# Kernel optimization log

Hardware: AMD Instinct MI355X
Metric: run time of the kernel (lower is better)

Reference implementation:

```python
import jax, jax.numpy as jnp
import numpy as np

B, D1, T = 256, 512, 256   # batch, input features, time steps
O1, O2 = 256, 128          # output features, output time/classes


def setup_inputs() -> dict:
    key = jax.random.key(0)
    ks = jax.random.split(key, 5)
    x = jax.random.normal(ks[0], (B, D1, T), dtype=jnp.float32)
    W1 = jax.random.normal(ks[1], (O1, D1), dtype=jnp.float32) / np.sqrt(D1).astype(np.float32)
    W = jax.random.normal(ks[2], (T, T), dtype=jnp.float32) / np.sqrt(T).astype(np.float32)
    W2 = jax.random.normal(ks[3], (T, O2), dtype=jnp.float32) / np.sqrt(T).astype(np.float32)
    alpha = jnp.array([0.5], dtype=jnp.float32)
    bias = jax.random.normal(ks[4], (O1, O2), dtype=jnp.float32) * 0.01
    return {"x": x, "W1": W1, "W": W, "W2": W2, "alpha": alpha, "bias": bias}


def reference(x, W1, W, W2, alpha, bias):
    # mode-1 product: project features. E: [B, O1, T]
    E = jnp.einsum('od,bdt->bot', W1, x)
    # temporal attention: softmax over time of E @ W. A: [B, O1, T]
    A = jax.nn.softmax(jnp.einsum('bot,ts->bos', E, W), axis=-1)
    a = alpha[0]
    blended = a * E + (1.0 - a) * E * A
    # mode-2 product: project time axis, add bias. Y: [B, O1, O2]
    Y = jnp.einsum('bot,ts->bos', blended, W2) + bias
    # per-sample softmax over the output-feature axis (torch.softmax(item4[i], 0))
    return jax.nn.softmax(Y, axis=1)
```

## Files before the change

kernel.cpp:

```cpp
#include <hip/hip_runtime.h>
#include <hip/hip_bf16.h>
#include <math.h>

#define B_   256
#define D1_  512
#define T_   256
#define O1_  256
#define O2_  128
#define OT   128

typedef __attribute__((ext_vector_type(8))) _Float16 f16x8;
typedef __attribute__((ext_vector_type(2))) _Float16 f16x2;
typedef __attribute__((ext_vector_type(4))) float f32x4;

__device__ inline unsigned pkh2(float a, float b) {
    union { f16x2 h; unsigned u; } c;
    c.h.x = (_Float16)a; c.h.y = (_Float16)b;
    return c.u;
}

__device__ inline void splith4(float v0, float v1, float v2, float v3,
                               uint2& hp, uint2& lp) {
    _Float16 h0 = (_Float16)v0, h1 = (_Float16)v1;
    _Float16 h2 = (_Float16)v2, h3 = (_Float16)v3;
    float r0 = v0 - (float)h0, r1 = v1 - (float)h1;
    float r2 = v2 - (float)h2, r3 = v3 - (float)h3;
    union { f16x2 h; unsigned u; } c;
    c.h.x = h0; c.h.y = h1; hp.x = c.u;
    c.h.x = h2; c.h.y = h3; hp.y = c.u;
    lp.x = pkh2(r0, r1); lp.y = pkh2(r2, r3);
}

__device__ inline uint2 cvth4(float v0, float v1, float v2, float v3) {
    uint2 r; r.x = pkh2(v0, v1); r.y = pkh2(v2, v3); return r;
}

__device__ inline f16x8 cvt8h(float4 a, float4 b) {
    f16x8 r;
    r[0] = (_Float16)a.x; r[1] = (_Float16)a.y;
    r[2] = (_Float16)a.z; r[3] = (_Float16)a.w;
    r[4] = (_Float16)b.x; r[5] = (_Float16)b.y;
    r[6] = (_Float16)b.z; r[7] = (_Float16)b.w;
    return r;
}

__device__ inline f16x8 ld16(const char* p) {
    union { uint2 a[2]; f16x8 v; } f;
    f.a[0] = *(const uint2*)p;
    f.a[1] = *(const uint2*)(p + 8);
    return f.v;
}
__device__ inline f16x8 ldb128(const char* p) { return *(const f16x8*)p; }

#define MFMAH __builtin_amdgcn_mfma_f32_16x16x32_f16

__global__ __launch_bounds__(1024, 4) void tabl_mfma(
    const float* __restrict__ x, const float* __restrict__ W1,
    const float* __restrict__ W, const float* __restrict__ W2,
    const float* __restrict__ alpha, const float* __restrict__ bias,
    float* __restrict__ out)
{
    __shared__ __align__(16) char Eh[OT * 512];
    __shared__ __align__(16) char Bst[2][2][256 * 72];
    __shared__ float redm[4][OT];
    __shared__ float reds[4][OT];

    const int tid    = threadIdx.x;
    const int lane16 = tid & 15;
    const int lg     = (tid >> 4) & 3;
    const int wid    = tid >> 6;
    const int wm     = wid >> 2;
    const int wn     = wid & 3;

    const int bi  = blockIdx.x;
    const int xcd = bi & 7, q = bi >> 3;
    const int b     = xcd + (q >> 1) * 8;
    const int obase = (q & 1) * OT;

    const int xs_t = tid & 255;
    const int koct = tid >> 8;
    const int stO  = xs_t * 72 + koct * 16;
    const int zs = tid & 127, zoct = (tid >> 7) & 7;
    const int stZ  = zs * 72 + zoct * 8;

    const int rArow[2] = { obase + wm * 32 + lane16, obase + wm * 32 + 16 + lane16 };
    const int eR[2]    = { wm * 32 + lane16, wm * 32 + 16 + lane16 };
    const int eBase[2] = { eR[0] * 512, eR[1] * 512 };
    const int eSw[2]   = { (eR[0] & 7) << 4, (eR[1] & 7) << 4 };
    int bOff[4], b3Off[2];
    #pragma unroll
    for (int nt = 0; nt < 4; ++nt) bOff[nt] = (wn * 64 + nt * 16 + lane16) * 72 + lg * 16;
    #pragma unroll
    for (int nt = 0; nt < 2; ++nt) b3Off[nt] = (wn * 32 + nt * 16 + lane16) * 72 + lg * 16;

    f32x4 Eacc[2][4];
    #pragma unroll
    for (int mt = 0; mt < 2; ++mt)
        #pragma unroll
        for (int nt = 0; nt < 4; ++nt) Eacc[mt][nt] = (f32x4){0.f,0.f,0.f,0.f};

    const float* xcol = x + (size_t)b * (D1_ * T_) + xs_t;
    float xr[8]; float4 apf[2][2];

    {
        #pragma unroll
        for (int j = 0; j < 8; ++j) xr[j] = xcol[(size_t)(koct * 8 + j) * T_];
        #pragma unroll
        for (int mt = 0; mt < 2; ++mt) {
            const float4* ap = (const float4*)(W1 + (size_t)rArow[mt] * D1_ + lg * 8);
            apf[mt][0] = ap[0]; apf[mt][1] = ap[1];
        }
        uint2 hp, lp;
        splith4(xr[0],xr[1],xr[2],xr[3],hp,lp);
        *(uint2*)(Bst[0][0] + stO) = hp; *(uint2*)(Bst[0][1] + stO) = lp;
        splith4(xr[4],xr[5],xr[6],xr[7],hp,lp);
        *(uint2*)(Bst[0][0] + stO + 8) = hp; *(uint2*)(Bst[0][1] + stO + 8) = lp;
    }
    __syncthreads();

    #pragma unroll 2
    for (int c = 0; c < 16; ++c) {
        const int cur = c & 1;
        if (c < 15) {
            #pragma unroll
            for (int j = 0; j < 8; ++j)
                xr[j] = xcol[(size_t)((c + 1) * 32 + koct * 8 + j) * T_];
        }
        f16x8 Ah[2];
        #pragma unroll
        for (int mt = 0; mt < 2; ++mt) Ah[mt] = cvt8h(apf[mt][0], apf[mt][1]);
        if (c < 15) {
            #pragma unroll
            for (int mt = 0; mt < 2; ++mt) {
                const float4* ap = (const float4*)(W1 + (size_t)rArow[mt] * D1_ + (c + 1) * 32 + lg * 8);
                apf[mt][0] = ap[0]; apf[mt][1] = ap[1];
            }
        }
        __builtin_amdgcn_s_setprio(1);
        #pragma unroll
        for (int np = 0; np < 2; ++np) {
            f16x8 Bh[2], Bl[2];
            #pragma unroll
            for (int h = 0; h < 2; ++h) {
                Bh[h] = ld16(Bst[cur][0] + bOff[np * 2 + h]);
                Bl[h] = ld16(Bst[cur][1] + bOff[np * 2 + h]);
            }
            #pragma unroll
            for (int mt = 0; mt < 2; ++mt)
                #pragma unroll
                for (int h = 0; h < 2; ++h) {
                    Eacc[mt][np*2+h] = MFMAH(Ah[mt], Bh[h], Eacc[mt][np*2+h], 0,0,0);
                    Eacc[mt][np*2+h] = MFMAH(Ah[mt], Bl[h], Eacc[mt][np*2+h], 0,0,0);
                }
        }
        __builtin_amdgcn_s_setprio(0);
        if (c < 15) {
            uint2 hp, lp;
            splith4(xr[0],xr[1],xr[2],xr[3],hp,lp);
            *(uint2*)(Bst[cur^1][0] + stO) = hp; *(uint2*)(Bst[cur^1][1] + stO) = lp;
            splith4(xr[4],xr[5],xr[6],xr[7],hp,lp);
            *(uint2*)(Bst[cur^1][0] + stO + 8) = hp; *(uint2*)(Bst[cur^1][1] + stO + 8) = lp;
        }
        __syncthreads();
    }

    #pragma unroll
    for (int mt = 0; mt < 2; ++mt)
        #pragma unroll
        for (int nt = 0; nt < 4; ++nt)
            #pragma unroll
            for (int i = 0; i < 4; ++i) {
                int r = wm * 32 + mt * 16 + lg * 4 + i;
                int t = wn * 64 + nt * 16 + lane16;
                union { _Float16 h; unsigned short u; } cc;
                cc.h = (_Float16)Eacc[mt][nt][i];
                *(unsigned short*)(Eh + r * 512 + ((2 * t) ^ ((r & 7) << 4))) = cc.u;
            }

    f32x4 Sacc[2][4];
    #pragma unroll
    for (int mt = 0; mt < 2; ++mt)
        #pragma unroll
        for (int nt = 0; nt < 4; ++nt) Sacc[mt][nt] = (f32x4){0.f,0.f,0.f,0.f};

    const float* wcol = W + xs_t;
    float wr[8];
    {
        #pragma unroll
        for (int j = 0; j < 8; ++j) wr[j] = wcol[(size_t)(koct * 8 + j) * T_];
        *(uint2*)(Bst[0][0] + stO)     = cvth4(wr[0],wr[1],wr[2],wr[3]);
        *(uint2*)(Bst[0][0] + stO + 8) = cvth4(wr[4],wr[5],wr[6],wr[7]);
    }
    __syncthreads();

    #pragma unroll 2
    for (int c = 0; c < 8; ++c) {
        const int cur = c & 1;
        if (c < 7) {
            #pragma unroll
            for (int j = 0; j < 8; ++j)
                wr[j] = wcol[(size_t)((c + 1) * 32 + koct * 8 + j) * T_];
        }
        f16x8 Af[2];
        #pragma unroll
        for (int mt = 0; mt < 2; ++mt)
            Af[mt] = ldb128(Eh + eBase[mt] + ((c * 64 + lg * 16) ^ eSw[mt]));
        __builtin_amdgcn_s_setprio(1);
        #pragma unroll
        for (int np = 0; np < 2; ++np) {
            f16x8 Bf[2];
            #pragma unroll
            for (int h = 0; h < 2; ++h) Bf[h] = ld16(Bst[cur][0] + bOff[np * 2 + h]);
            #pragma unroll
            for (int mt = 0; mt < 2; ++mt)
                #pragma unroll
                for (int h = 0; h < 2; ++h)
                    Sacc[mt][np*2+h] = MFMAH(Af[mt], Bf[h], Sacc[mt][np*2+h], 0,0,0);
        }
        __builtin_amdgcn_s_setprio(0);
        if (c < 7) {
            *(uint2*)(Bst[cur^1][0] + stO)     = cvth4(wr[0],wr[1],wr[2],wr[3]);
            *(uint2*)(Bst[cur^1][0] + stO + 8) = cvth4(wr[4],wr[5],wr[6],wr[7]);
        }
        __syncthreads();
    }

    const float a_ = alpha[0];
    float pm[2][4];
    #pragma unroll
    for (int mt = 0; mt < 2; ++mt)
        #pragma unroll
        for (int i = 0; i < 4; ++i) {
            float m = fmaxf(fmaxf(Sacc[mt][0][i], Sacc[mt][1][i]),
                            fmaxf(Sacc[mt][2][i], Sacc[mt][3][i]));
            m = fmaxf(m, __shfl_xor(m, 1));
            m = fmaxf(m, __shfl_xor(m, 2));
            m = fmaxf(m, __shfl_xor(m, 4));
            m = fmaxf(m, __shfl_xor(m, 8));
            float s = 0.f;
            #pragma unroll
            for (int nt = 0; nt < 4; ++nt) {
                float p = __expf(Sacc[mt][nt][i] - m);
                Sacc[mt][nt][i] = p; s += p;
            }
            s += __shfl_xor(s, 1);
            s += __shfl_xor(s, 2);
            s += __shfl_xor(s, 4);
            s += __shfl_xor(s, 8);
            pm[mt][i] = m;
            if (lane16 == 0) {
                int r = wm * 32 + mt * 16 + lg * 4 + i;
                redm[wn][r] = m; reds[wn][r] = s;
            }
        }
    float zr[4];
    #pragma unroll
    for (int j = 0; j < 4; ++j) zr[j] = W2[(size_t)(zoct * 4 + j) * O2_ + zs];
    __syncthreads();

    #pragma unroll
    for (int mt = 0; mt < 2; ++mt)
        #pragma unroll
        for (int i = 0; i < 4; ++i) {
            int r = wm * 32 + mt * 16 + lg * 4 + i;
            float M = fmaxf(fmaxf(redm[0][r], redm[1][r]),
                            fmaxf(redm[2][r], redm[3][r]));
            float den = reds[0][r] * __expf(redm[0][r] - M)
                      + reds[1][r] * __expf(redm[1][r] - M)
                      + reds[2][r] * __expf(redm[2][r] - M)
                      + reds[3][r] * __expf(redm[3][r] - M);
            float sc = __expf(pm[mt][i] - M) / den;
            #pragma unroll
            for (int nt = 0; nt < 4; ++nt) {
                float f = a_ + (1.f - a_) * Sacc[mt][nt][i] * sc;
                float v = Eacc[mt][nt][i] * f;
                int t = wn * 64 + nt * 16 + lane16;
                union { _Float16 h; unsigned short u; } cc;
                cc.h = (_Float16)v;
                *(unsigned short*)(Eh + r * 512 + ((2 * t) ^ ((r & 7) << 4))) = cc.u;
            }
        }
    {
        *(uint2*)(Bst[0][0] + stZ) = cvth4(zr[0], zr[1], zr[2], zr[3]);
    }
    __syncthreads();

    f32x4 Yacc[2][2];
    #pragma unroll
    for (int mt = 0; mt < 2; ++mt)
        #pragma unroll
        for (int nt = 0; nt < 2; ++nt) Yacc[mt][nt] = (f32x4){0.f,0.f,0.f,0.f};

    #pragma unroll 2
    for (int c = 0; c < 8; ++c) {
        const int cur = c & 1;
        if (c < 7) {
            #pragma unroll
            for (int j = 0; j < 4; ++j)
                zr[j] = W2[(size_t)((c + 1) * 32 + zoct * 4 + j) * O2_ + zs];
        }
        f16x8 Ahf[2];
        #pragma unroll
        for (int mt = 0; mt < 2; ++mt)
            Ahf[mt] = ldb128(Eh + eBase[mt] + ((c * 64 + lg * 16) ^ eSw[mt]));
        __builtin_amdgcn_s_setprio(1);
        {
            f16x8 Bh[2];
            #pragma unroll
            for (int nt = 0; nt < 2; ++nt) Bh[nt] = ld16(Bst[cur][0] + b3Off[nt]);
            #pragma unroll
            for (int mt = 0; mt < 2; ++mt)
                #pragma unroll
                for (int nt = 0; nt < 2; ++nt)
                    Yacc[mt][nt] = MFMAH(Ahf[mt], Bh[nt], Yacc[mt][nt], 0,0,0);
        }
        __builtin_amdgcn_s_setprio(0);
        if (c < 7) {
            *(uint2*)(Bst[cur^1][0] + stZ) = cvth4(zr[0], zr[1], zr[2], zr[3]);
        }
        __syncthreads();
    }

    #pragma unroll
    for (int mt = 0; mt < 2; ++mt)
        #pragma unroll
        for (int nt = 0; nt < 2; ++nt)
            #pragma unroll
            for (int i = 0; i < 4; ++i) {
                int o  = obase + wm * 32 + mt * 16 + lg * 4 + i;
                int s2 = wn * 32 + nt * 16 + lane16;
                out[((size_t)b * O1_ + o) * O2_ + s2] =
                    Yacc[mt][nt][i] + bias[(size_t)o * O2_ + s2];
            }
}

__global__ __launch_bounds__(256) void softmax_o1(float* __restrict__ out)
{
    __shared__ float sm[2][128], ss[2][128];
    const int b  = blockIdx.x;
    const int s2 = threadIdx.x & 127;
    const int oh = threadIdx.x >> 7;
    float* p = out + (size_t)b * (O1_ * O2_) + s2;
    float m = -INFINITY, s = 0.f;
    #pragma unroll 4
    for (int o = oh * 128; o < oh * 128 + 128; ++o) {
        float v = p[(size_t)o * O2_];
        float mn = fmaxf(m, v);
        s = s * __expf(m - mn) + __expf(v - mn);
        m = mn;
    }
    sm[oh][s2] = m; ss[oh][s2] = s;
    __syncthreads();
    float M = fmaxf(sm[0][s2], sm[1][s2]);
    float S = ss[0][s2] * __expf(sm[0][s2] - M) + ss[1][s2] * __expf(sm[1][s2] - M);
    float inv = 1.f / S;
    #pragma unroll 4
    for (int o = oh * 128; o < oh * 128 + 128; ++o) {
        float v = p[(size_t)o * O2_];
        p[(size_t)o * O2_] = __expf(v - M) * inv;
    }
}

extern "C" void kernel_launch(void* const* d_in, const int* in_sizes, int n_in,
                              void* d_out, int out_size, void* d_ws, size_t ws_size,
                              hipStream_t stream)
{
    const float* x     = (const float*)d_in[0];
    const float* W1    = (const float*)d_in[1];
    const float* W     = (const float*)d_in[2];
    const float* W2    = (const float*)d_in[3];
    const float* alpha = (const float*)d_in[4];
    const float* bias  = (const float*)d_in[5];
    float* out = (float*)d_out;

    tabl_mfma<<<dim3(512), 1024, 0, stream>>>(x, W1, W, W2, alpha, bias, out);
    softmax_o1<<<B_, 256, 0, stream>>>(out);
}
```

Before: 139.8 us.

## Prefetch global operands two chunks ahead across all three GEMM stages

Deepens the software pipeline in the three GEMM loops (x/W1 projection, E@W scores, blended@W2). Global loads for chunk c+2 are now issued while chunk c is computed, and the LDS store of the already-loaded chunk c+1 happens at the top of the iteration instead of after the MFMAs. This is meant to hide more global memory latency behind MFMA work. The cost is more live registers for the extra prefetch buffers, which could lower occupancy.

```diff
diff --git a/kernel.cpp b/kernel.cpp
--- a/kernel.cpp
+++ b/kernel.cpp
@@ -100,20 +100,23 @@
         for (int nt = 0; nt < 4; ++nt) Eacc[mt][nt] = (f32x4){0.f,0.f,0.f,0.f};
 
     const float* xcol = x + (size_t)b * (D1_ * T_) + xs_t;
-    float xr[8]; float4 apf[2][2];
+    float xrN[8]; float4 apfC[2][2], apfN[2][2];
 
     {
-        #pragma unroll
-        for (int j = 0; j < 8; ++j) xr[j] = xcol[(size_t)(koct * 8 + j) * T_];
+        float x0[8];
+        #pragma unroll
+        for (int j = 0; j < 8; ++j) x0[j] = xcol[(size_t)(koct * 8 + j) * T_];
         #pragma unroll
         for (int mt = 0; mt < 2; ++mt) {
             const float4* ap = (const float4*)(W1 + (size_t)rArow[mt] * D1_ + lg * 8);
-            apf[mt][0] = ap[0]; apf[mt][1] = ap[1];
-        }
+            apfC[mt][0] = ap[0]; apfC[mt][1] = ap[1];
+        }
+        #pragma unroll
+        for (int j = 0; j < 8; ++j) xrN[j] = xcol[(size_t)(32 + koct * 8 + j) * T_];
         uint2 hp, lp;
-        splith4(xr[0],xr[1],xr[2],xr[3],hp,lp);
+        splith4(x0[0],x0[1],x0[2],x0[3],hp,lp);
         *(uint2*)(Bst[0][0] + stO) = hp; *(uint2*)(Bst[0][1] + stO) = lp;
-        splith4(xr[4],xr[5],xr[6],xr[7],hp,lp);
+        splith4(x0[4],x0[5],x0[6],x0[7],hp,lp);
         *(uint2*)(Bst[0][0] + stO + 8) = hp; *(uint2*)(Bst[0][1] + stO + 8) = lp;
     }
     __syncthreads();
@@ -122,18 +125,25 @@
     for (int c = 0; c < 16; ++c) {
         const int cur = c & 1;
         if (c < 15) {
+            uint2 hp, lp;
+            splith4(xrN[0],xrN[1],xrN[2],xrN[3],hp,lp);
+            *(uint2*)(Bst[cur^1][0] + stO) = hp; *(uint2*)(Bst[cur^1][1] + stO) = lp;
+            splith4(xrN[4],xrN[5],xrN[6],xrN[7],hp,lp);
+            *(uint2*)(Bst[cur^1][0] + stO + 8) = hp; *(uint2*)(Bst[cur^1][1] + stO + 8) = lp;
+        }
+        if (c < 14) {
             #pragma unroll
             for (int j = 0; j < 8; ++j)
-                xr[j] = xcol[(size_t)((c + 1) * 32 + koct * 8 + j) * T_];
+                xrN[j] = xcol[(size_t)((c + 2) * 32 + koct * 8 + j) * T_];
         }
         f16x8 Ah[2];
         #pragma unroll
-        for (int mt = 0; mt < 2; ++mt) Ah[mt] = cvt8h(apf[mt][0], apf[mt][1]);
+        for (int mt = 0; mt < 2; ++mt) Ah[mt] = cvt8h(apfC[mt][0], apfC[mt][1]);
         if (c < 15) {
             #pragma unroll
             for (int mt = 0; mt < 2; ++mt) {
                 const float4* ap = (const float4*)(W1 + (size_t)rArow[mt] * D1_ + (c + 1) * 32 + lg * 8);
-                apf[mt][0] = ap[0]; apf[mt][1] = ap[1];
+                apfN[mt][0] = ap[0]; apfN[mt][1] = ap[1];
             }
         }
         __builtin_amdgcn_s_setprio(1);
@@ -154,12 +164,9 @@
                 }
         }
         __builtin_amdgcn_s_setprio(0);
-        if (c < 15) {
-            uint2 hp, lp;
-            splith4(xr[0],xr[1],xr[2],xr[3],hp,lp);
-            *(uint2*)(Bst[cur^1][0] + stO) = hp; *(uint2*)(Bst[cur^1][1] + stO) = lp;
-            splith4(xr[4],xr[5],xr[6],xr[7],hp,lp);
-            *(uint2*)(Bst[cur^1][0] + stO + 8) = hp; *(uint2*)(Bst[cur^1][1] + stO + 8) = lp;
+        #pragma unroll
+        for (int mt = 0; mt < 2; ++mt) {
+            apfC[mt][0] = apfN[mt][0]; apfC[mt][1] = apfN[mt][1];
         }
         __syncthreads();
     }
@@ -184,12 +191,15 @@
         for (int nt = 0; nt < 4; ++nt) Sacc[mt][nt] = (f32x4){0.f,0.f,0.f,0.f};
 
     const float* wcol = W + xs_t;
-    float wr[8];
+    float wrN[8];
     {
-        #pragma unroll
-        for (int j = 0; j < 8; ++j) wr[j] = wcol[(size_t)(koct * 8 + j) * T_];
-        *(uint2*)(Bst[0][0] + stO)     = cvth4(wr[0],wr[1],wr[2],wr[3]);
-        *(uint2*)(Bst[0][0] + stO + 8) = cvth4(wr[4],wr[5],wr[6],wr[7]);
+        float w0[8];
+        #pragma unroll
+        for (int j = 0; j < 8; ++j) w0[j] = wcol[(size_t)(koct * 8 + j) * T_];
+        #pragma unroll
+        for (int j = 0; j < 8; ++j) wrN[j] = wcol[(size_t)(32 + koct * 8 + j) * T_];
+        *(uint2*)(Bst[0][0] + stO)     = cvth4(w0[0],w0[1],w0[2],w0[3]);
+        *(uint2*)(Bst[0][0] + stO + 8) = cvth4(w0[4],w0[5],w0[6],w0[7]);
     }
     __syncthreads();
 
@@ -197,9 +207,13 @@
     for (int c = 0; c < 8; ++c) {
         const int cur = c & 1;
         if (c < 7) {
+            *(uint2*)(Bst[cur^1][0] + stO)     = cvth4(wrN[0],wrN[1],wrN[2],wrN[3]);
+            *(uint2*)(Bst[cur^1][0] + stO + 8) = cvth4(wrN[4],wrN[5],wrN[6],wrN[7]);
+        }
+        if (c < 6) {
             #pragma unroll
             for (int j = 0; j < 8; ++j)
-                wr[j] = wcol[(size_t)((c + 1) * 32 + koct * 8 + j) * T_];
+                wrN[j] = wcol[(size_t)((c + 2) * 32 + koct * 8 + j) * T_];
         }
         f16x8 Af[2];
         #pragma unroll
@@ -218,10 +232,6 @@
                     Sacc[mt][np*2+h] = MFMAH(Af[mt], Bf[h], Sacc[mt][np*2+h], 0,0,0);
         }
         __builtin_amdgcn_s_setprio(0);
-        if (c < 7) {
-            *(uint2*)(Bst[cur^1][0] + stO)     = cvth4(wr[0],wr[1],wr[2],wr[3]);
-            *(uint2*)(Bst[cur^1][0] + stO + 8) = cvth4(wr[4],wr[5],wr[6],wr[7]);
-        }
         __syncthreads();
     }
 
@@ -253,9 +263,11 @@
                 redm[wn][r] = m; reds[wn][r] = s;
             }
         }
-    float zr[4];
-    #pragma unroll
-    for (int j = 0; j < 4; ++j) zr[j] = W2[(size_t)(zoct * 4 + j) * O2_ + zs];
+    float zr0[4], zrN[4];
+    #pragma unroll
+    for (int j = 0; j < 4; ++j) zr0[j] = W2[(size_t)(zoct * 4 + j) * O2_ + zs];
+    #pragma unroll
+    for (int j = 0; j < 4; ++j) zrN[j] = W2[(size_t)(32 + zoct * 4 + j) * O2_ + zs];
     __syncthreads();
 
     #pragma unroll
@@ -281,7 +293,7 @@
             }
         }
     {
-        *(uint2*)(Bst[0][0] + stZ) = cvth4(zr[0], zr[1], zr[2], zr[3]);
+        *(uint2*)(Bst[0][0] + stZ) = cvth4(zr0[0], zr0[1], zr0[2], zr0[3]);
     }
     __syncthreads();
 
@@ -295,9 +307,12 @@
     for (int c = 0; c < 8; ++c) {
         const int cur = c & 1;
         if (c < 7) {
+            *(uint2*)(Bst[cur^1][0] + stZ) = cvth4(zrN[0], zrN[1], zrN[2], zrN[3]);
+        }
+        if (c < 6) {
             #pragma unroll
             for (int j = 0; j < 4; ++j)
-                zr[j] = W2[(size_t)((c + 1) * 32 + zoct * 4 + j) * O2_ + zs];
+                zrN[j] = W2[(size_t)((c + 2) * 32 + zoct * 4 + j) * O2_ + zs];
         }
         f16x8 Ahf[2];
         #pragma unroll
@@ -315,9 +330,6 @@
                     Yacc[mt][nt] = MFMAH(Ahf[mt], Bh[nt], Yacc[mt][nt], 0,0,0);
         }
         __builtin_amdgcn_s_setprio(0);
-        if (c < 7) {
-            *(uint2*)(Bst[cur^1][0] + stZ) = cvth4(zr[0], zr[1], zr[2], zr[3]);
-        }
         __syncthreads();
     }
 
```

New measurement: 147.4 us. 1.05x slower.

## Drop split-fp16 x compensation and halve per-block output rows

Applied to the files above, without the earlier changes.

The first GEMM no longer splits x into high and low fp16 halves, so the second compensating MFMA and its staging buffer are removed. Each block now covers 64 output rows with 512 threads over 1024 blocks, which halves shared memory per block and changes the occupancy and work split. The blend step reads E back from shared memory instead of from the accumulator registers. This cuts MFMA work and register pressure, but with 1024 blocks each batch's x slice is reloaded by four blocks instead of two, and dropping the compensation lowers the precision of E.

```diff
diff --git a/kernel.cpp b/kernel.cpp
--- a/kernel.cpp
+++ b/kernel.cpp
@@ -7,43 +7,24 @@
 #define T_   256
 #define O1_  256
 #define O2_  128
-#define OT   128
+#define OT   64
 
 typedef __attribute__((ext_vector_type(8))) _Float16 f16x8;
-typedef __attribute__((ext_vector_type(2))) _Float16 f16x2;
 typedef __attribute__((ext_vector_type(4))) float f32x4;
 
 __device__ inline unsigned pkh2(float a, float b) {
-    union { f16x2 h; unsigned u; } c;
-    c.h.x = (_Float16)a; c.h.y = (_Float16)b;
-    return c.u;
-}
-
-__device__ inline void splith4(float v0, float v1, float v2, float v3,
-                               uint2& hp, uint2& lp) {
-    _Float16 h0 = (_Float16)v0, h1 = (_Float16)v1;
-    _Float16 h2 = (_Float16)v2, h3 = (_Float16)v3;
-    float r0 = v0 - (float)h0, r1 = v1 - (float)h1;
-    float r2 = v2 - (float)h2, r3 = v3 - (float)h3;
-    union { f16x2 h; unsigned u; } c;
-    c.h.x = h0; c.h.y = h1; hp.x = c.u;
-    c.h.x = h2; c.h.y = h3; hp.y = c.u;
-    lp.x = pkh2(r0, r1); lp.y = pkh2(r2, r3);
-}
-
+    union { _Float16 h[2]; unsigned u; } c;
+    c.h[0] = (_Float16)a; c.h[1] = (_Float16)b; return c.u;
+}
 __device__ inline uint2 cvth4(float v0, float v1, float v2, float v3) {
     uint2 r; r.x = pkh2(v0, v1); r.y = pkh2(v2, v3); return r;
 }
-
-__device__ inline f16x8 cvt8h(float4 a, float4 b) {
+__device__ inline f16x8 cvt8h(const float* v) {
     f16x8 r;
-    r[0] = (_Float16)a.x; r[1] = (_Float16)a.y;
-    r[2] = (_Float16)a.z; r[3] = (_Float16)a.w;
-    r[4] = (_Float16)b.x; r[5] = (_Float16)b.y;
-    r[6] = (_Float16)b.z; r[7] = (_Float16)b.w;
+    #pragma unroll
+    for (int j = 0; j < 8; ++j) r[j] = (_Float16)v[j];
     return r;
 }
-
 __device__ inline f16x8 ld16(const char* p) {
     union { uint2 a[2]; f16x8 v; } f;
     f.a[0] = *(const uint2*)p;
@@ -54,14 +35,14 @@
 
 #define MFMAH __builtin_amdgcn_mfma_f32_16x16x32_f16
 
-__global__ __launch_bounds__(1024, 4) void tabl_mfma(
+__global__ __launch_bounds__(512, 4) void tabl_mfma(
     const float* __restrict__ x, const float* __restrict__ W1,
     const float* __restrict__ W, const float* __restrict__ W2,
     const float* __restrict__ alpha, const float* __restrict__ bias,
     float* __restrict__ out)
 {
     __shared__ __align__(16) char Eh[OT * 512];
-    __shared__ __align__(16) char Bst[2][2][256 * 72];
+    __shared__ __align__(16) char Bst[2][256 * 72];
     __shared__ float redm[4][OT];
     __shared__ float reds[4][OT];
 
@@ -72,16 +53,16 @@
     const int wm     = wid >> 2;
     const int wn     = wid & 3;
 
-    const int bi  = blockIdx.x;
-    const int xcd = bi & 7, q = bi >> 3;
-    const int b     = xcd + (q >> 1) * 8;
-    const int obase = (q & 1) * OT;
-
-    const int xs_t = tid & 255;
-    const int koct = tid >> 8;
-    const int stO  = xs_t * 72 + koct * 16;
-    const int zs = tid & 127, zoct = (tid >> 7) & 7;
-    const int stZ  = zs * 72 + zoct * 8;
+    const int bid = blockIdx.x;
+    const int idx = bid >> 3;
+    const int b     = (bid & 7) + 8 * (idx >> 2);
+    const int obase = (idx & 3) * OT;
+
+    const int xs_t  = tid & 255;
+    const int xs_kh = tid >> 8;
+    const int stO   = xs_t * 72 + xs_kh * 32;
+    const int zs = tid & 127, zq = (tid >> 7) & 3;
+    const int stZ   = zs * 72 + zq * 16;
 
     const int rArow[2] = { obase + wm * 32 + lane16, obase + wm * 32 + 16 + lane16 };
     const int eR[2]    = { wm * 32 + lane16, wm * 32 + 16 + lane16 };
@@ -100,21 +81,23 @@
         for (int nt = 0; nt < 4; ++nt) Eacc[mt][nt] = (f32x4){0.f,0.f,0.f,0.f};
 
     const float* xcol = x + (size_t)b * (D1_ * T_) + xs_t;
-    float xr[8]; float4 apf[2][2];
+    float xn[16];
+    f16x8 AhC[2];
 
     {
-        #pragma unroll
-        for (int j = 0; j < 8; ++j) xr[j] = xcol[(size_t)(koct * 8 + j) * T_];
+        float x0[16];
+        #pragma unroll
+        for (int j = 0; j < 16; ++j) x0[j] = xcol[(size_t)(xs_kh * 16 + j) * T_];
         #pragma unroll
         for (int mt = 0; mt < 2; ++mt) {
-            const float4* ap = (const float4*)(W1 + (size_t)rArow[mt] * D1_ + lg * 8);
-            apf[mt][0] = ap[0]; apf[mt][1] = ap[1];
-        }
-        uint2 hp, lp;
-        splith4(xr[0],xr[1],xr[2],xr[3],hp,lp);
-        *(uint2*)(Bst[0][0] + stO) = hp; *(uint2*)(Bst[0][1] + stO) = lp;
-        splith4(xr[4],xr[5],xr[6],xr[7],hp,lp);
-        *(uint2*)(Bst[0][0] + stO + 8) = hp; *(uint2*)(Bst[0][1] + stO + 8) = lp;
+            float av[8];
+            *(float4*)&av[0] = *(const float4*)(W1 + (size_t)rArow[mt] * D1_ + lg * 8);
+            *(float4*)&av[4] = *(const float4*)(W1 + (size_t)rArow[mt] * D1_ + lg * 8 + 4);
+            AhC[mt] = cvt8h(av);
+        }
+        #pragma unroll
+        for (int q = 0; q < 4; ++q)
+            *(uint2*)(Bst[0] + stO + q * 8) = cvth4(x0[q*4+0], x0[q*4+1], x0[q*4+2], x0[q*4+3]);
     }
     __syncthreads();
 
@@ -123,43 +106,37 @@
         const int cur = c & 1;
         if (c < 15) {
             #pragma unroll
-            for (int j = 0; j < 8; ++j)
-                xr[j] = xcol[(size_t)((c + 1) * 32 + koct * 8 + j) * T_];
-        }
-        f16x8 Ah[2];
-        #pragma unroll
-        for (int mt = 0; mt < 2; ++mt) Ah[mt] = cvt8h(apf[mt][0], apf[mt][1]);
+            for (int j = 0; j < 16; ++j)
+                xn[j] = xcol[(size_t)((c + 1) * 32 + xs_kh * 16 + j) * T_];
+        }
+        float4 apN[2][2];
         if (c < 15) {
             #pragma unroll
             for (int mt = 0; mt < 2; ++mt) {
                 const float4* ap = (const float4*)(W1 + (size_t)rArow[mt] * D1_ + (c + 1) * 32 + lg * 8);
-                apf[mt][0] = ap[0]; apf[mt][1] = ap[1];
+                apN[mt][0] = ap[0]; apN[mt][1] = ap[1];
             }
         }
         __builtin_amdgcn_s_setprio(1);
         #pragma unroll
-        for (int np = 0; np < 2; ++np) {
-            f16x8 Bh[2], Bl[2];
-            #pragma unroll
-            for (int h = 0; h < 2; ++h) {
-                Bh[h] = ld16(Bst[cur][0] + bOff[np * 2 + h]);
-                Bl[h] = ld16(Bst[cur][1] + bOff[np * 2 + h]);
-            }
+        for (int nt = 0; nt < 4; ++nt) {
+            f16x8 Bh = ld16(Bst[cur] + bOff[nt]);
             #pragma unroll
             for (int mt = 0; mt < 2; ++mt)
-                #pragma unroll
-                for (int h = 0; h < 2; ++h) {
-                    Eacc[mt][np*2+h] = MFMAH(Ah[mt], Bh[h], Eacc[mt][np*2+h], 0,0,0);
-                    Eacc[mt][np*2+h] = MFMAH(Ah[mt], Bl[h], Eacc[mt][np*2+h], 0,0,0);
-                }
+                Eacc[mt][nt] = MFMAH(AhC[mt], Bh, Eacc[mt][nt], 0,0,0);
         }
         __builtin_amdgcn_s_setprio(0);
         if (c < 15) {
-            uint2 hp, lp;
-            splith4(xr[0],xr[1],xr[2],xr[3],hp,lp);
-            *(uint2*)(Bst[cur^1][0] + stO) = hp; *(uint2*)(Bst[cur^1][1] + stO) = lp;
-            splith4(xr[4],xr[5],xr[6],xr[7],hp,lp);
-            *(uint2*)(Bst[cur^1][0] + stO + 8) = hp; *(uint2*)(Bst[cur^1][1] + stO + 8) = lp;
+            #pragma unroll
+            for (int q = 0; q < 4; ++q)
+                *(uint2*)(Bst[cur^1] + stO + q * 8) = cvth4(xn[q*4+0], xn[q*4+1], xn[q*4+2], xn[q*4+3]);
+            #pragma unroll
+            for (int mt = 0; mt < 2; ++mt) {
+                float av[8];
+                *(float4*)&av[0] = apN[mt][0];
+                *(float4*)&av[4] = apN[mt][1];
+                AhC[mt] = cvt8h(av);
+            }
         }
         __syncthreads();
     }
@@ -184,22 +161,24 @@
         for (int nt = 0; nt < 4; ++nt) Sacc[mt][nt] = (f32x4){0.f,0.f,0.f,0.f};
 
     const float* wcol = W + xs_t;
-    float wr[8];
     {
-        #pragma unroll
-        for (int j = 0; j < 8; ++j) wr[j] = wcol[(size_t)(koct * 8 + j) * T_];
-        *(uint2*)(Bst[0][0] + stO)     = cvth4(wr[0],wr[1],wr[2],wr[3]);
-        *(uint2*)(Bst[0][0] + stO + 8) = cvth4(wr[4],wr[5],wr[6],wr[7]);
-    }
-    __syncthreads();
-
+        float w0[16];
+        #pragma unroll
+        for (int j = 0; j < 16; ++j) w0[j] = wcol[(size_t)(xs_kh * 16 + j) * T_];
+        #pragma unroll
+        for (int q = 0; q < 4; ++q)
+            *(uint2*)(Bst[0] + stO + q * 8) = cvth4(w0[q*4+0], w0[q*4+1], w0[q*4+2], w0[q*4+3]);
+    }
+    __syncthreads();
+
+    float wv[16];
     #pragma unroll 2
     for (int c = 0; c < 8; ++c) {
         const int cur = c & 1;
         if (c < 7) {
             #pragma unroll
-            for (int j = 0; j < 8; ++j)
-                wr[j] = wcol[(size_t)((c + 1) * 32 + koct * 8 + j) * T_];
+            for (int j = 0; j < 16; ++j)
+                wv[j] = wcol[(size_t)((c + 1) * 32 + xs_kh * 16 + j) * T_];
         }
         f16x8 Af[2];
         #pragma unroll
@@ -207,20 +186,17 @@
             Af[mt] = ldb128(Eh + eBase[mt] + ((c * 64 + lg * 16) ^ eSw[mt]));
         __builtin_amdgcn_s_setprio(1);
         #pragma unroll
-        for (int np = 0; np < 2; ++np) {
-            f16x8 Bf[2];
-            #pragma unroll
-            for (int h = 0; h < 2; ++h) Bf[h] = ld16(Bst[cur][0] + bOff[np * 2 + h]);
+        for (int nt = 0; nt < 4; ++nt) {
+            f16x8 Bf = ld16(Bst[cur] + bOff[nt]);
             #pragma unroll
             for (int mt = 0; mt < 2; ++mt)
-                #pragma unroll
-                for (int h = 0; h < 2; ++h)
-                    Sacc[mt][np*2+h] = MFMAH(Af[mt], Bf[h], Sacc[mt][np*2+h], 0,0,0);
+                Sacc[mt][nt] = MFMAH(Af[mt], Bf, Sacc[mt][nt], 0,0,0);
         }
         __builtin_amdgcn_s_setprio(0);
         if (c < 7) {
-            *(uint2*)(Bst[cur^1][0] + stO)     = cvth4(wr[0],wr[1],wr[2],wr[3]);
-            *(uint2*)(Bst[cur^1][0] + stO + 8) = cvth4(wr[4],wr[5],wr[6],wr[7]);
+            #pragma unroll
+            for (int q = 0; q < 4; ++q)
+                *(uint2*)(Bst[cur^1] + stO + q * 8) = cvth4(wv[q*4+0], wv[q*4+1], wv[q*4+2], wv[q*4+3]);
         }
         __syncthreads();
     }
@@ -253,9 +229,6 @@
                 redm[wn][r] = m; reds[wn][r] = s;
             }
         }
-    float zr[4];
-    #pragma unroll
-    for (int j = 0; j < 4; ++j) zr[j] = W2[(size_t)(zoct * 4 + j) * O2_ + zs];
     __syncthreads();
 
     #pragma unroll
@@ -273,15 +246,20 @@
             #pragma unroll
             for (int nt = 0; nt < 4; ++nt) {
                 float f = a_ + (1.f - a_) * Sacc[mt][nt][i] * sc;
-                float v = Eacc[mt][nt][i] * f;
                 int t = wn * 64 + nt * 16 + lane16;
+                int off = r * 512 + ((2 * t) ^ ((r & 7) << 4));
                 union { _Float16 h; unsigned short u; } cc;
-                cc.h = (_Float16)v;
-                *(unsigned short*)(Eh + r * 512 + ((2 * t) ^ ((r & 7) << 4))) = cc.u;
+                cc.u = *(const unsigned short*)(Eh + off);
+                cc.h = (_Float16)((float)cc.h * f);
+                *(unsigned short*)(Eh + off) = cc.u;
             }
         }
     {
-        *(uint2*)(Bst[0][0] + stZ) = cvth4(zr[0], zr[1], zr[2], zr[3]);
+        float z0[8];
+        #pragma unroll
+        for (int j = 0; j < 8; ++j) z0[j] = W2[(size_t)(zq * 8 + j) * O2_ + zs];
+        *(uint2*)(Bst[0] + stZ)     = cvth4(z0[0], z0[1], z0[2], z0[3]);
+        *(uint2*)(Bst[0] + stZ + 8) = cvth4(z0[4], z0[5], z0[6], z0[7]);
     }
     __syncthreads();
 
@@ -291,32 +269,31 @@
         #pragma unroll
         for (int nt = 0; nt < 2; ++nt) Yacc[mt][nt] = (f32x4){0.f,0.f,0.f,0.f};
 
+    float zv[8];
     #pragma unroll 2
     for (int c = 0; c < 8; ++c) {
         const int cur = c & 1;
         if (c < 7) {
             #pragma unroll
-            for (int j = 0; j < 4; ++j)
-                zr[j] = W2[(size_t)((c + 1) * 32 + zoct * 4 + j) * O2_ + zs];
-        }
-        f16x8 Ahf[2];
+            for (int j = 0; j < 8; ++j)
+                zv[j] = W2[(size_t)((c + 1) * 32 + zq * 8 + j) * O2_ + zs];
+        }
+        f16x8 Af[2];
         #pragma unroll
         for (int mt = 0; mt < 2; ++mt)
-            Ahf[mt] = ldb128(Eh + eBase[mt] + ((c * 64 + lg * 16) ^ eSw[mt]));
+            Af[mt] = ldb128(Eh + eBase[mt] + ((c * 64 + lg * 16) ^ eSw[mt]));
         __builtin_amdgcn_s_setprio(1);
-        {
-            f16x8 Bh[2];
-            #pragma unroll
-            for (int nt = 0; nt < 2; ++nt) Bh[nt] = ld16(Bst[cur][0] + b3Off[nt]);
+        #pragma unroll
+        for (int nt = 0; nt < 2; ++nt) {
+            f16x8 Bf = ld16(Bst[cur] + b3Off[nt]);
             #pragma unroll
             for (int mt = 0; mt < 2; ++mt)
-                #pragma unroll
-                for (int nt = 0; nt < 2; ++nt)
-                    Yacc[mt][nt] = MFMAH(Ahf[mt], Bh[nt], Yacc[mt][nt], 0,0,0);
+                Yacc[mt][nt] = MFMAH(Af[mt], Bf, Yacc[mt][nt], 0,0,0);
         }
         __builtin_amdgcn_s_setprio(0);
         if (c < 7) {
-            *(uint2*)(Bst[cur^1][0] + stZ) = cvth4(zr[0], zr[1], zr[2], zr[3]);
+            *(uint2*)(Bst[cur^1] + stZ)     = cvth4(zv[0], zv[1], zv[2], zv[3]);
+            *(uint2*)(Bst[cur^1] + stZ + 8) = cvth4(zv[4], zv[5], zv[6], zv[7]);
         }
         __syncthreads();
     }
@@ -373,6 +350,6 @@
     const float* bias  = (const float*)d_in[5];
     float* out = (float*)d_out;
 
-    tabl_mfma<<<dim3(512), 1024, 0, stream>>>(x, W1, W, W2, alpha, bias, out);
+    tabl_mfma<<<dim3(1024), 512, 0, stream>>>(x, W1, W, W2, alpha, bias, out);
     softmax_o1<<<B_, 256, 0, stream>>>(out);
 }
```

Measured after the change: 143.6 us. 1.03x slower.
